# Kernel tuning notes

Measured on AMD Instinct MI355X. Metric: run time of the kernel, lower is better.

Reference implementation:

```python
import jax, jax.numpy as jnp
import numpy as np

EPS = 1e-5
K_UP = 5      # k_upsample
SCALE = 2

def _conv(x, w, pad):
    # NCHW conv, no bias
    return jax.lax.conv_general_dilated(
        x, w, window_strides=(1, 1), padding=((pad, pad), (pad, pad)),
        dimension_numbers=('NCHW', 'OIHW', 'NCHW'))

def _bn(x, gamma, beta):
    # train-mode BatchNorm2d forward: batch stats over (N,H,W), biased var
    m = x.mean(axis=(0, 2, 3), keepdims=True)
    v = x.var(axis=(0, 2, 3), keepdims=True)
    xn = (x - m) * jax.lax.rsqrt(v + EPS)
    return xn * gamma[None, :, None, None] + beta[None, :, None, None]

def _pixel_shuffle(x, r):
    b, c, h, w = x.shape
    co = c // (r * r)
    x = x.reshape(b, co, r, r, h, w)
    x = x.transpose(0, 1, 4, 2, 5, 3)  # b, co, h, r, w, r
    return x.reshape(b, co, h * r, w * r)

def setup_inputs() -> dict:
    key = jax.random.key(0)
    ks = jax.random.split(key, 3)
    b, c, h, w = 8, 128, 64, 64
    mid = 64
    return {
        'x': jax.random.normal(ks[0], (b, c, h, w), jnp.float32),
        'comp_w': jax.random.normal(ks[1], (mid, c, 1, 1), jnp.float32) * (1.0 / np.sqrt(c)),
        'comp_g': jnp.ones((mid,), jnp.float32),
        'comp_b': jnp.zeros((mid,), jnp.float32),
        'enc_w': jax.random.normal(ks[2], ((K_UP * SCALE) ** 2, mid, 3, 3), jnp.float32) * (1.0 / np.sqrt(mid * 9)),
        'enc_g': jnp.ones(((K_UP * SCALE) ** 2,), jnp.float32),
        'enc_b': jnp.zeros(((K_UP * SCALE) ** 2,), jnp.float32),
    }

def reference(x, comp_w, comp_g, comp_b, enc_w, enc_g, enc_b):
    b, c, h, w = x.shape
    hm, wm = h * SCALE, w * SCALE
    # --- kernel prediction branch ---
    t = jax.nn.silu(_bn(_conv(x, comp_w, 0), comp_g, comp_b))        # [b,64,h,w]
    t = _bn(_conv(t, enc_w, 1), enc_g, enc_b)                        # [b,100,h,w] (act=False)
    t = _pixel_shuffle(t, SCALE)                                     # [b,25,hm,wm]
    wgt = jax.nn.softmax(t, axis=1)                                  # [b,25,hm,wm]
    # --- feature reassembly branch ---
    x_up = jnp.repeat(jnp.repeat(x, SCALE, axis=2), SCALE, axis=3)   # nearest upsample
    pad = (K_UP // 2) * SCALE  # = 4, preserves hm x wm with dilation=SCALE
    xp = jnp.pad(x_up, ((0, 0), (0, 0), (pad, pad), (pad, pad)))
    # unfold: kernel K_UP, dilation SCALE -> [b, c, 25, hm, wm], taps in (kh, kw) order
    patches = jnp.stack(
        [xp[:, :, dy * SCALE:dy * SCALE + hm, dx * SCALE:dx * SCALE + wm]
         for dy in range(K_UP) for dx in range(K_UP)], axis=2)
    # content-aware weighted sum over the 25 taps
    return jnp.einsum('bkhw,bckhw->bchw', wgt, patches)
```

## Files before the change

kernel.cpp:

```cpp
#include <hip/hip_runtime.h>
#include <hip/hip_bf16.h>
#include <math.h>

#define C_   128
#define HW_  4096
#define OC_  100
#define NSTAT_ 32768.0f

typedef __bf16 bf16x8 __attribute__((ext_vector_type(8)));
typedef __bf16 bf16x4 __attribute__((ext_vector_type(4)));
typedef float  f32x4  __attribute__((ext_vector_type(4)));

__global__ __launch_bounds__(256, 4) void k_conv1(const float* __restrict__ x,
                                                  const float* __restrict__ w,
                                                  const float* __restrict__ wenc,
                                                  __bf16* __restrict__ t1c,
                                                  float* __restrict__ csum,
                                                  float* __restrict__ csq,
                                                  __bf16* __restrict__ wprep) {
    __shared__ __bf16 xt[64 * 128];
    __shared__ __bf16 wt[64 * 128];
    __shared__ float sS[64], sQ[64];

    int blk = blockIdx.x;
    int b = blk & 7;
    int chunk = blk >> 3;
    int px0 = chunk * 64;
    int tid = threadIdx.x;
    if (tid < 64) { sS[tid] = 0.f; sQ[tid] = 0.f; }

    if (blk < 63) {
#pragma unroll
        for (int u = 0; u < 4; ++u) {
            int idx = blk * 1024 + u * 256 + tid;
            int oc = idx / 576, k = idx - oc * 576;
            int tap = k >> 6, ic = k & 63;
            wprep[idx] = (oc < OC_) ? (__bf16)wenc[((size_t)oc * 64 + ic) * 9 + tap]
                                    : (__bf16)0.f;
        }
    }

#pragma unroll
    for (int it = 0; it < 8; ++it) {
        int j = it * 256 + tid;
        int oc = j >> 5, f = j & 31;
        float4 v = *(const float4*)(w + (size_t)oc * 128 + f * 4);
        int blki = (f >> 1) ^ (oc & 15);
        bf16x4 st;
        st[0] = (__bf16)v.x; st[1] = (__bf16)v.y; st[2] = (__bf16)v.z; st[3] = (__bf16)v.w;
        *(bf16x4*)&wt[oc * 128 + blki * 8 + (f & 1) * 4] = st;
    }
#pragma unroll
    for (int it = 0; it < 2; ++it) {
        int j = it * 256 + tid;
        int px4 = (j & 15) * 4, icq = j >> 4;
        const float* xp = x + ((size_t)b * C_ + icq * 4) * HW_ + px0 + px4;
        float4 v0 = *(const float4*)(xp);
        float4 v1 = *(const float4*)(xp + HW_);
        float4 v2 = *(const float4*)(xp + 2 * HW_);
        float4 v3 = *(const float4*)(xp + 3 * HW_);
        float r0[4] = {v0.x, v0.y, v0.z, v0.w};
        float r1[4] = {v1.x, v1.y, v1.z, v1.w};
        float r2_[4] = {v2.x, v2.y, v2.z, v2.w};
        float r3[4] = {v3.x, v3.y, v3.z, v3.w};
#pragma unroll
        for (int r2 = 0; r2 < 4; ++r2) {
            int px = px4 + r2;
            int blki = (icq >> 1) ^ (px & 15);
            bf16x4 st;
            st[0] = (__bf16)r0[r2]; st[1] = (__bf16)r1[r2];
            st[2] = (__bf16)r2_[r2]; st[3] = (__bf16)r3[r2];
            *(bf16x4*)&xt[px * 128 + blki * 8 + (icq & 1) * 4] = st;
        }
    }
    __syncthreads();

    int lane = tid & 63, wv = tid >> 6;
    int p = lane & 15, q = lane >> 4;

    f32x4 acc[4];
#pragma unroll
    for (int n = 0; n < 4; ++n) acc[n] = (f32x4){0.f, 0.f, 0.f, 0.f};

#pragma unroll
    for (int kk = 0; kk < 4; ++kk) {
        int blki = (kk * 4 + q) ^ p;
        bf16x8 a = *(const bf16x8*)&xt[(wv * 16 + p) * 128 + blki * 8];
#pragma unroll
        for (int n = 0; n < 4; ++n) {
            bf16x8 bb = *(const bf16x8*)&wt[(n * 16 + p) * 128 + blki * 8];
            acc[n] = __builtin_amdgcn_mfma_f32_16x16x32_bf16(a, bb, acc[n], 0, 0, 0);
        }
    }

    __bf16* t1b = t1c + ((size_t)b * HW_ + px0 + wv * 16) * 64;
#pragma unroll
    for (int n = 0; n < 4; ++n) {
        float s = 0.f, qq = 0.f;
#pragma unroll
        for (int rg = 0; rg < 4; ++rg) {
            float v = acc[n][rg];
            t1b[(size_t)(q * 4 + rg) * 64 + n * 16 + p] = (__bf16)v;
            s += v; qq += v * v;
        }
        s += __shfl_down(s, 32, 64);  s += __shfl_down(s, 16, 64);
        qq += __shfl_down(qq, 32, 64); qq += __shfl_down(qq, 16, 64);
        if (lane < 16) {
            atomicAdd(&sS[n * 16 + p], s);
            atomicAdd(&sQ[n * 16 + p], qq);
        }
    }
    __syncthreads();
    if (tid < 64) {
        atomicAdd(&csum[tid], sS[tid]);
        atomicAdd(&csq[tid], sQ[tid]);
    }
}

__global__ __launch_bounds__(256, 4) void k_conv3(const __bf16* __restrict__ t1c,
                                                  const __bf16* __restrict__ wprep,
                                                  const float* __restrict__ csum,
                                                  const float* __restrict__ csq,
                                                  const float* __restrict__ cg,
                                                  const float* __restrict__ cb,
                                                  float* __restrict__ t2c,
                                                  float* __restrict__ esum,
                                                  float* __restrict__ esq) {
    __shared__ float xtf[25 * 260];
    __bf16* xt = (__bf16*)xtf;
    __shared__ float lsc[64], lsh[64];
    __shared__ float esuml[112], esql[112];

    int blk = blockIdx.x;
    int b = blk & 7;
    int tile = blk >> 3;
    int ty0 = (tile >> 3) * 8, tx0 = (tile & 7) * 8;
    int tid = threadIdx.x;
    if (tid < 112) { esuml[tid] = 0.f; esql[tid] = 0.f; }
    if (tid >= 128 && tid < 192) {
        int c = tid - 128;
        float invN = 1.0f / NSTAT_;
        float m = csum[c] * invN;
        float v = csq[c] * invN - m * m;
        float rs = rsqrtf(v + 1e-5f);
        float sc = cg[c] * rs;
        lsc[c] = sc;
        lsh[c] = cb[c] - m * sc;
    }
    __syncthreads();

    const __bf16* tb = t1c + (size_t)b * HW_ * 64;
#pragma unroll
    for (int it = 0; it < 7; ++it) {
        int idx = it * 256 + tid;
        if (idx < 1600) {
            int pxi = idx >> 4, f4 = idx & 15;
            int yy = pxi / 10, xx = pxi - yy * 10;
            int gy = ty0 + yy - 1, gx = tx0 + xx - 1;
            float o0 = 0.f, o1 = 0.f, o2 = 0.f, o3 = 0.f;
            if (gy >= 0 && gy < 64 && gx >= 0 && gx < 64) {
                bf16x4 v = *(const bf16x4*)(tb + ((size_t)(gy << 6) + gx) * 64 + f4 * 4);
                float4 sc = *(const float4*)(lsc + f4 * 4);
                float4 sh = *(const float4*)(lsh + f4 * 4);
                float u;
                u = fmaf((float)v[0], sc.x, sh.x); o0 = u / (1.f + __expf(-u));
                u = fmaf((float)v[1], sc.y, sh.y); o1 = u / (1.f + __expf(-u));
                u = fmaf((float)v[2], sc.z, sh.z); o2 = u / (1.f + __expf(-u));
                u = fmaf((float)v[3], sc.w, sh.w); o3 = u / (1.f + __expf(-u));
            }
            bf16x4 st;
            st[0] = (__bf16)o0; st[1] = (__bf16)o1; st[2] = (__bf16)o2; st[3] = (__bf16)o3;
            *(bf16x4*)&xt[pxi * 72 + f4 * 4] = st;
        }
    }
    __syncthreads();

    int lane = tid & 63, wv = tid >> 6;
    int p = lane & 15, q = lane >> 4;
    int ya = 2 * wv + (p >> 3), xa = p & 7;
    const __bf16* wpl = wprep + p * 576 + q * 8;

    f32x4 acc[7];
#pragma unroll
    for (int n = 0; n < 7; ++n) acc[n] = (f32x4){0.f, 0.f, 0.f, 0.f};

#pragma unroll
    for (int kk = 0; kk < 18; ++kk) {
        const int tap = kk >> 1, ich = (kk & 1) * 32;
        const int ky = tap / 3, kx = tap - ky * 3;
        bf16x8 a0 = *(const bf16x8*)&xt[((ya + ky) * 10 + xa + kx) * 72 + ich + q * 8];
#pragma unroll
        for (int n = 0; n < 7; ++n) {
            bf16x8 bb = *(const bf16x8*)(wpl + n * 9216 + kk * 32);
            acc[n] = __builtin_amdgcn_mfma_f32_16x16x32_bf16(a0, bb, acc[n], 0, 0, 0);
        }
    }
    __syncthreads();

#pragma unroll
    for (int n = 0; n < 7; ++n) {
        int oc = n * 16 + p;
        int k5 = oc >> 2, sch = oc & 3;
        bool wr = oc < OC_;
        float s = 0.f, qq = 0.f;
#pragma unroll
        for (int rg = 0; rg < 4; ++rg) {
            int mp = q * 4 + rg;
            float v = acc[n][rg];
            if (wr) xtf[k5 * 260 + (2 * wv + (mp >> 3)) * 32 + (mp & 7) * 4 + sch] = v;
            s += v; qq += v * v;
        }
        s += __shfl_down(s, 32, 64);  s += __shfl_down(s, 16, 64);
        qq += __shfl_down(qq, 32, 64); qq += __shfl_down(qq, 16, 64);
        if (lane < 16) {
            atomicAdd(&esuml[n * 16 + lane], s);
            atomicAdd(&esql[n * 16 + lane], qq);
        }
    }
    __syncthreads();

    float* t2b = t2c + (size_t)b * 25 * HW_ * 4;
#pragma unroll
    for (int it = 0; it < 7; ++it) {
        int idx = it * 256 + tid;
        if (idx < 1600) {
            int k5 = idx >> 6, pix = idx & 63;
            f32x4 v = *(const f32x4*)&xtf[k5 * 260 + pix * 4];
            int gy = ty0 + (pix >> 3), gx = tx0 + (pix & 7);
            *(f32x4*)&t2b[((size_t)k5 * HW_ + (gy << 6) + gx) * 4] = v;
        }
    }
    if (tid < 112) {
        atomicAdd(&esum[tid], esuml[tid]);
        atomicAdd(&esq[tid], esql[tid]);
    }
}

__global__ __launch_bounds__(512, 2) void k_carafe(const float* __restrict__ x,
                                                   const float* __restrict__ t2c,
                                                   const float* __restrict__ esum,
                                                   const float* __restrict__ esq,
                                                   const float* __restrict__ eg,
                                                   const float* __restrict__ eb,
                                                   float* __restrict__ out) {
    __shared__ float xt[400 * 20];
    __shared__ float esc[112], esh[112];

    int blk = blockIdx.x;
    int b = blk & 7;
    int r = blk >> 3;
    int tile = r & 15;
    int cq = r >> 4;
    int tx0 = (tile & 3) * 16, ty0 = (tile >> 2) * 16;
    int tid = threadIdx.x;
    if (tid < 112) {
        float invN = 1.0f / NSTAT_;
        float m = esum[tid] * invN;
        float v = esq[tid] * invN - m * m;
        float rs = rsqrtf(v + 1e-5f);
        float sc = (tid < OC_) ? eg[tid] * rs : 0.f;
        esc[tid] = sc;
        esh[tid] = (tid < OC_) ? eb[tid] - m * sc : 0.f;
    }

    int t0 = tid & 1, px = tid >> 1;
    int pxx = px & 15, py = px >> 4;
    int iy = ty0 + py, jx = tx0 + pxx;
    int pxl = (iy << 6) + jx;

    const float* xb = x + (size_t)b * C_ * HW_;

    f32x4 pf[4];
#pragma unroll
    for (int it = 0; it < 4; ++it) {
        int idx = it * 512 + tid;
        if (idx < 1600) {
            int c4 = idx / 400;
            int hp = idx - c4 * 400;
            int yy = hp / 20, xx = hp - yy * 20;
            int gy = ty0 - 2 + yy, gx = tx0 - 2 + xx;
            f32x4 st = {0.f, 0.f, 0.f, 0.f};
            if (gy >= 0 && gy < 64 && gx >= 0 && gx < 64) {
                size_t base = (size_t)(cq * 32 + c4 * 4) * HW_ + (gy << 6) + gx;
                st[0] = xb[base];
                st[1] = xb[base + HW_];
                st[2] = xb[base + 2 * HW_];
                st[3] = xb[base + 3 * HW_];
            }
            pf[it] = st;
        }
    }
    __syncthreads();

    float wA[25], wB[25];
    {
        const float* t2p = t2c + (size_t)b * 25 * HW_ * 4 + (size_t)pxl * 4 + 2 * t0;
        int cA = 2 * t0, cB = 2 * t0 + 1;
        float mxA = -1e30f, mxB = -1e30f;
#pragma unroll
        for (int k = 0; k < 25; ++k) {
            float2 v = *(const float2*)(t2p + (size_t)k * HW_ * 4);
            float lA = fmaf(v.x, esc[4 * k + cA], esh[4 * k + cA]);
            float lB = fmaf(v.y, esc[4 * k + cB], esh[4 * k + cB]);
            wA[k] = lA; wB[k] = lB;
            mxA = fmaxf(mxA, lA); mxB = fmaxf(mxB, lB);
        }
        float sA = 0.f, sB = 0.f;
#pragma unroll
        for (int k = 0; k < 25; ++k) {
            float eA = __expf(wA[k] - mxA);
            float eB = __expf(wB[k] - mxB);
            wA[k] = eA; wB[k] = eB;
            sA += eA; sB += eB;
        }
        float iA = 1.f / sA, iB = 1.f / sB;
#pragma unroll
        for (int k = 0; k < 25; ++k) { wA[k] *= iA; wB[k] *= iB; }
    }

#pragma unroll
    for (int it = 0; it < 4; ++it) {
        int idx = it * 512 + tid;
        if (idx < 1600) {
            int c4 = idx / 400;
            int hp = idx - c4 * 400;
            *(f32x4*)&xt[hp * 20 + c4 * 4] = pf[it];
        }
    }
    __syncthreads();

    int i0 = iy * 2 + t0;
    float* op = out + (size_t)b * C_ * 16384 + (size_t)i0 * 128 + jx * 2;
    int cbase = cq * 32;

    f32x4 pg[4];
#pragma unroll
    for (int it = 0; it < 4; ++it) {
        int idx = it * 512 + tid;
        if (idx < 1600) {
            int c4 = idx / 400;
            int hp = idx - c4 * 400;
            int yy = hp / 20, xx = hp - yy * 20;
            int gy = ty0 - 2 + yy, gx = tx0 - 2 + xx;
            f32x4 st = {0.f, 0.f, 0.f, 0.f};
            if (gy >= 0 && gy < 64 && gx >= 0 && gx < 64) {
                size_t base = (size_t)(cbase + 16 + c4 * 4) * HW_ + (gy << 6) + gx;
                st[0] = xb[base];
                st[1] = xb[base + HW_];
                st[2] = xb[base + 2 * HW_];
                st[3] = xb[base + 3 * HW_];
            }
            pg[it] = st;
        }
    }

    {
        float accA[16], accB[16];
#pragma unroll
        for (int e = 0; e < 16; ++e) { accA[e] = 0.f; accB[e] = 0.f; }
#pragma unroll
        for (int dy = 0; dy < 5; ++dy)
#pragma unroll
            for (int dx = 0; dx < 5; ++dx) {
                int pos = (py + dy) * 20 + pxx + dx;
                float a = wA[dy * 5 + dx], bw = wB[dy * 5 + dx];
#pragma unroll
                for (int c4 = 0; c4 < 4; ++c4) {
                    f32x4 xv = *(const f32x4*)&xt[pos * 20 + c4 * 4];
                    accA[c4 * 4 + 0] = fmaf(a, xv[0], accA[c4 * 4 + 0]);
                    accA[c4 * 4 + 1] = fmaf(a, xv[1], accA[c4 * 4 + 1]);
                    accA[c4 * 4 + 2] = fmaf(a, xv[2], accA[c4 * 4 + 2]);
                    accA[c4 * 4 + 3] = fmaf(a, xv[3], accA[c4 * 4 + 3]);
                    accB[c4 * 4 + 0] = fmaf(bw, xv[0], accB[c4 * 4 + 0]);
                    accB[c4 * 4 + 1] = fmaf(bw, xv[1], accB[c4 * 4 + 1]);
                    accB[c4 * 4 + 2] = fmaf(bw, xv[2], accB[c4 * 4 + 2]);
                    accB[c4 * 4 + 3] = fmaf(bw, xv[3], accB[c4 * 4 + 3]);
                }
            }
#pragma unroll
        for (int e = 0; e < 16; ++e) {
            float2 st2;
            st2.x = accA[e]; st2.y = accB[e];
            *(float2*)&op[(size_t)(cbase + e) * 16384] = st2;
        }
    }
    __syncthreads();

#pragma unroll
    for (int it = 0; it < 4; ++it) {
        int idx = it * 512 + tid;
        if (idx < 1600) {
            int c4 = idx / 400;
            int hp = idx - c4 * 400;
            *(f32x4*)&xt[hp * 20 + c4 * 4] = pg[it];
        }
    }
    __syncthreads();

    {
        float accA[16], accB[16];
#pragma unroll
        for (int e = 0; e < 16; ++e) { accA[e] = 0.f; accB[e] = 0.f; }
#pragma unroll
        for (int dy = 0; dy < 5; ++dy)
#pragma unroll
            for (int dx = 0; dx < 5; ++dx) {
                int pos = (py + dy) * 20 + pxx + dx;
                float a = wA[dy * 5 + dx], bw = wB[dy * 5 + dx];
#pragma unroll
                for (int c4 = 0; c4 < 4; ++c4) {
                    f32x4 xv = *(const f32x4*)&xt[pos * 20 + c4 * 4];
                    accA[c4 * 4 + 0] = fmaf(a, xv[0], accA[c4 * 4 + 0]);
                    accA[c4 * 4 + 1] = fmaf(a, xv[1], accA[c4 * 4 + 1]);
                    accA[c4 * 4 + 2] = fmaf(a, xv[2], accA[c4 * 4 + 2]);
                    accA[c4 * 4 + 3] = fmaf(a, xv[3], accA[c4 * 4 + 3]);
                    accB[c4 * 4 + 0] = fmaf(bw, xv[0], accB[c4 * 4 + 0]);
                    accB[c4 * 4 + 1] = fmaf(bw, xv[1], accB[c4 * 4 + 1]);
                    accB[c4 * 4 + 2] = fmaf(bw, xv[2], accB[c4 * 4 + 2]);
                    accB[c4 * 4 + 3] = fmaf(bw, xv[3], accB[c4 * 4 + 3]);
                }
            }
#pragma unroll
        for (int e = 0; e < 16; ++e) {
            float2 st2;
            st2.x = accA[e]; st2.y = accB[e];
            *(float2*)&op[(size_t)(cbase + 16 + e) * 16384] = st2;
        }
    }
}

extern "C" void kernel_launch(void* const* d_in, const int* in_sizes, int n_in,
                              void* d_out, int out_size, void* d_ws, size_t ws_size,
                              hipStream_t stream) {
    const float* x      = (const float*)d_in[0];
    const float* comp_w = (const float*)d_in[1];
    const float* comp_g = (const float*)d_in[2];
    const float* comp_b = (const float*)d_in[3];
    const float* enc_w  = (const float*)d_in[4];
    const float* enc_g  = (const float*)d_in[5];
    const float* enc_b  = (const float*)d_in[6];
    float* out = (float*)d_out;

    float* ws = (float*)d_ws;
    __bf16* t1c = (__bf16*)ws;
    float* t2c  = ws + 1048576;
    float* st   = ws + 1048576 + 3670016;
    float* csum = st;
    float* csq  = st + 64;
    float* esum = st + 128;
    float* esq  = st + 240;
    __bf16* wprep = (__bf16*)(st + 352);

    hipMemsetAsync(st, 0, 352 * sizeof(float), stream);
    k_conv1<<<512, 256, 0, stream>>>(x, comp_w, enc_w, t1c, csum, csq, wprep);
    k_conv3<<<512, 256, 0, stream>>>(t1c, wprep, csum, csq, comp_g, comp_b, t2c, esum, esq);
    k_carafe<<<512, 512, 0, stream>>>(x, t2c, esum, esq, enc_g, enc_b, out);
}
```

Measured before the change: 177.3 us.

## Split conv3 output channels across two blocks and stage weights in LDS

The 3x3 encoder conv kernel now launches twice as many blocks, with each block computing half of the output channels (64 or 48) for its 8x8 tile. This aims to raise parallelism and cut per-thread accumulator registers. Weights are double-buffered through shared memory per k-step instead of being read directly from global memory, adding a barrier each iteration. In exchange, the halo tile load and SiLU/BN recomputation are duplicated across the two halves.

```diff
diff --git a/kernel.cpp b/kernel.cpp
--- a/kernel.cpp
+++ b/kernel.cpp
@@ -126,16 +126,24 @@
                                                   float* __restrict__ t2c,
                                                   float* __restrict__ esum,
                                                   float* __restrict__ esq) {
-    __shared__ float xtf[25 * 260];
-    __bf16* xt = (__bf16*)xtf;
+    __shared__ float shbuf[6160];
+    __bf16* xt  = (__bf16*)shbuf;
+    __bf16* btb = (__bf16*)((char*)shbuf + 14400);
+    float*  xtf = shbuf;
     __shared__ float lsc[64], lsh[64];
     __shared__ float esuml[112], esql[112];
 
     int blk = blockIdx.x;
     int b = blk & 7;
-    int tile = blk >> 3;
+    int rest = blk >> 3;
+    int tile = rest & 63;
+    int half = rest >> 6;
     int ty0 = (tile >> 3) * 8, tx0 = (tile & 7) * 8;
     int tid = threadIdx.x;
+    const int oc0 = half * 64;
+    const int NOC = half ? 48 : 64;
+    const int NT  = half ? 3 : 4;
+
     if (tid < 112) { esuml[tid] = 0.f; esql[tid] = 0.f; }
     if (tid >= 128 && tid < 192) {
         int c = tid - 128;
@@ -147,6 +155,13 @@
         lsc[c] = sc;
         lsh[c] = cb[c] - m * sc;
     }
+
+    int soc = tid >> 2, spart = tid & 3;
+    bool sact = soc < NOC;
+    int sdst = soc * 40 + spart * 8;
+    const __bf16* wsrc = wprep + (size_t)(oc0 + soc) * 576 + spart * 8;
+
+    if (sact) *(bf16x8*)&btb[sdst] = *(const bf16x8*)(wsrc);
     __syncthreads();
 
     const __bf16* tb = t1c + (size_t)b * HW_ * 64;
@@ -178,59 +193,73 @@
     int lane = tid & 63, wv = tid >> 6;
     int p = lane & 15, q = lane >> 4;
     int ya = 2 * wv + (p >> 3), xa = p & 7;
-    const __bf16* wpl = wprep + p * 576 + q * 8;
-
-    f32x4 acc[7];
-#pragma unroll
-    for (int n = 0; n < 7; ++n) acc[n] = (f32x4){0.f, 0.f, 0.f, 0.f};
+
+    f32x4 acc[4];
+#pragma unroll
+    for (int n = 0; n < 4; ++n) acc[n] = (f32x4){0.f, 0.f, 0.f, 0.f};
 
 #pragma unroll
     for (int kk = 0; kk < 18; ++kk) {
+        const int cur = kk & 1;
+        bf16x8 r0;
+        if (kk < 17 && sact) r0 = *(const bf16x8*)(wsrc + (kk + 1) * 32);
         const int tap = kk >> 1, ich = (kk & 1) * 32;
         const int ky = tap / 3, kx = tap - ky * 3;
         bf16x8 a0 = *(const bf16x8*)&xt[((ya + ky) * 10 + xa + kx) * 72 + ich + q * 8];
-#pragma unroll
-        for (int n = 0; n < 7; ++n) {
-            bf16x8 bb = *(const bf16x8*)(wpl + n * 9216 + kk * 32);
-            acc[n] = __builtin_amdgcn_mfma_f32_16x16x32_bf16(a0, bb, acc[n], 0, 0, 0);
-        }
-    }
-    __syncthreads();
-
-#pragma unroll
-    for (int n = 0; n < 7; ++n) {
-        int oc = n * 16 + p;
-        int k5 = oc >> 2, sch = oc & 3;
-        bool wr = oc < OC_;
-        float s = 0.f, qq = 0.f;
-#pragma unroll
-        for (int rg = 0; rg < 4; ++rg) {
-            int mp = q * 4 + rg;
-            float v = acc[n][rg];
-            if (wr) xtf[k5 * 260 + (2 * wv + (mp >> 3)) * 32 + (mp & 7) * 4 + sch] = v;
-            s += v; qq += v * v;
-        }
-        s += __shfl_down(s, 32, 64);  s += __shfl_down(s, 16, 64);
-        qq += __shfl_down(qq, 32, 64); qq += __shfl_down(qq, 16, 64);
-        if (lane < 16) {
-            atomicAdd(&esuml[n * 16 + lane], s);
-            atomicAdd(&esql[n * 16 + lane], qq);
-        }
-    }
-    __syncthreads();
-
+        const __bf16* btc = btb + cur * 2560;
+#pragma unroll
+        for (int n = 0; n < 4; ++n) {
+            if (n < NT) {
+                bf16x8 bb = *(const bf16x8*)&btc[(n * 16 + p) * 40 + q * 8];
+                acc[n] = __builtin_amdgcn_mfma_f32_16x16x32_bf16(a0, bb, acc[n], 0, 0, 0);
+            }
+        }
+        if (kk < 17) {
+            if (sact) *(bf16x8*)&btb[(1 - cur) * 2560 + sdst] = r0;
+            __syncthreads();
+        }
+    }
+    __syncthreads();
+
+#pragma unroll
+    for (int n = 0; n < 4; ++n) {
+        if (n < NT) {
+            int ocl = n * 16 + p;
+            int oc = oc0 + ocl;
+            int k5l = ocl >> 2, sch = ocl & 3;
+            bool wr = oc < OC_;
+            float s = 0.f, qq = 0.f;
+#pragma unroll
+            for (int rg = 0; rg < 4; ++rg) {
+                int mp = q * 4 + rg;
+                float v = acc[n][rg];
+                if (wr) xtf[k5l * 260 + (2 * wv + (mp >> 3)) * 32 + (mp & 7) * 4 + sch] = v;
+                s += v; qq += v * v;
+            }
+            s += __shfl_down(s, 32, 64);  s += __shfl_down(s, 16, 64);
+            qq += __shfl_down(qq, 32, 64); qq += __shfl_down(qq, 16, 64);
+            if (lane < 16) {
+                atomicAdd(&esuml[oc0 + n * 16 + lane], s);
+                atomicAdd(&esql[oc0 + n * 16 + lane], qq);
+            }
+        }
+    }
+    __syncthreads();
+
+    const int NK5 = half ? 9 : 16;
+    const int jobs = NK5 * 64;
     float* t2b = t2c + (size_t)b * 25 * HW_ * 4;
 #pragma unroll
-    for (int it = 0; it < 7; ++it) {
+    for (int it = 0; it < 4; ++it) {
         int idx = it * 256 + tid;
-        if (idx < 1600) {
-            int k5 = idx >> 6, pix = idx & 63;
-            f32x4 v = *(const f32x4*)&xtf[k5 * 260 + pix * 4];
+        if (idx < jobs) {
+            int k5l = idx >> 6, pix = idx & 63;
+            f32x4 v = *(const f32x4*)&xtf[k5l * 260 + pix * 4];
             int gy = ty0 + (pix >> 3), gx = tx0 + (pix & 7);
-            *(f32x4*)&t2b[((size_t)k5 * HW_ + (gy << 6) + gx) * 4] = v;
-        }
-    }
-    if (tid < 112) {
+            *(f32x4*)&t2b[((size_t)(half * 16 + k5l) * HW_ + (gy << 6) + gx) * 4] = v;
+        }
+    }
+    if (tid >= oc0 && tid < oc0 + NOC) {
         atomicAdd(&esum[tid], esuml[tid]);
         atomicAdd(&esq[tid], esql[tid]);
     }
@@ -453,6 +482,6 @@
 
     hipMemsetAsync(st, 0, 352 * sizeof(float), stream);
     k_conv1<<<512, 256, 0, stream>>>(x, comp_w, enc_w, t1c, csum, csq, wprep);
-    k_conv3<<<512, 256, 0, stream>>>(t1c, wprep, csum, csq, comp_g, comp_b, t2c, esum, esq);
+    k_conv3<<<1024, 256, 0, stream>>>(t1c, wprep, csum, csq, comp_g, comp_b, t2c, esum, esq);
     k_carafe<<<512, 512, 0, stream>>>(x, t2c, esum, esq, enc_g, enc_b, out);
 }
```

After: 158.6 us. -10.5%, faster.
